# Performance work log

Hardware: AMD Instinct MI355X
Metric: run time of the kernel (lower is better)

The kernel has to match this reference:

```python
import jax, jax.numpy as jnp
import numpy as np

B, N, D = 8, 1024, 1024

def setup_inputs() -> dict:
    key = jax.random.key(0)
    k1, k2, k3, k4, k5 = jax.random.split(key, 5)
    x = jax.random.normal(k1, (B, N, D), dtype=jnp.float32)
    y = jax.random.normal(k2, (B, N, D), dtype=jnp.float32)
    adj = jax.random.uniform(k3, (B, N, N), dtype=jnp.float32)
    adj_sumrow = jnp.sum(adj, axis=-1, keepdims=True)  # [B, N, 1], row-sum normalizer
    W = jax.random.normal(k4, (D, D), dtype=jnp.float32) * (1.0 / np.sqrt(D))
    b = jax.random.normal(k5, (D,), dtype=jnp.float32) * 0.02
    return {"x": x, "y": y, "adj": adj, "adj_sumrow": adj_sumrow, "W": W, "b": b}

def reference(x, y, adj, adj_sumrow, W, b):
    # GraphConvolutionCustom: project neighbor features, aggregate via dense adj,
    # normalize by row-sum, add bias and residual input x; then ReLU.
    # Dropout is identity in eval mode (training=False).
    support = jnp.einsum('bnd,de->bne', y, W)          # [B, N, D]
    agg = jnp.matmul(adj, support) / adj_sumrow        # [B, N, D]
    out = jax.nn.relu(agg + b + x)
    return out
```

## Files before the change

### kernel.cpp

```cpp
#include <hip/hip_runtime.h>
#include <hip/hip_bf16.h>
#include <stdint.h>


typedef float  f32x4  __attribute__((ext_vector_type(4)));
typedef __bf16 bf16x8 __attribute__((ext_vector_type(8)));

__device__ __forceinline__ unsigned short f2bf(float f) {
  union { float f; unsigned int u; } c; c.f = f;
  unsigned int u = c.u;
  u += 0x7FFFu + ((u >> 16) & 1u);
  return (unsigned short)(u >> 16);
}

__device__ __forceinline__ void async_cp16(const void* g, void* l) {
  __builtin_amdgcn_global_load_lds(
      (const __attribute__((address_space(1))) unsigned int*)g,
      (__attribute__((address_space(3))) unsigned int*)l, 16, 0, 0);
}

__device__ __forceinline__ void bar() { asm volatile("s_barrier" ::: "memory"); }
#define VMCNT(n) asm volatile("s_waitcnt vmcnt(" #n ")" ::: "memory")


__global__ __launch_bounds__(256) void k_prep(
    const float4* __restrict__ y4, const float4* __restrict__ a4,
    ushort4* __restrict__ yb, ushort4* __restrict__ ab,
    const float* __restrict__ W, unsigned short* __restrict__ Wt)
{
  __shared__ float t[64][65];
  const int bid = blockIdx.x;
  if (bid < 16384) {
    const int i = bid * 256 + threadIdx.x;
    const bool isY = i < 2097152;
    const float4 v = isY ? y4[i] : a4[i - 2097152];
    ushort4 p;
    p.x = f2bf(v.x); p.y = f2bf(v.y); p.z = f2bf(v.z); p.w = f2bf(v.w);
    if (isY) yb[i] = p; else ab[i - 2097152] = p;
  } else {
    const int id = bid - 16384;
    const int n0 = (id & 15) * 64, k0 = (id >> 4) * 64;
    const int tx = threadIdx.x & 63, ty = threadIdx.x >> 6;
#pragma unroll
    for (int r = ty; r < 64; r += 4)
      t[r][tx] = W[(size_t)(k0 + r) * 1024 + n0 + tx];
    __syncthreads();
#pragma unroll
    for (int r = ty; r < 64; r += 4)
      Wt[(size_t)(n0 + r) * 1024 + k0 + tx] = f2bf(t[tx][r]);
  }
}


__device__ __forceinline__ void stageA(
    const unsigned short* __restrict__ A, int sA, int m0, int k0, int c,
    unsigned short* la, int wave, int rg, int colo)
{
#pragma unroll
  for (int s = 0; s < 2; ++s) {
    const int t = wave * 2 + s;
    const int row0 = (t >> 2) * 64 + c * 32 + (t & 3) * 8;
    async_cp16(A + (size_t)(m0 + row0 + rg) * sA + k0 + colo, la + row0 * 64);
  }
}

__device__ __forceinline__ void stageB(
    const unsigned short* __restrict__ Bt, int sB, int n0, int k0,
    unsigned short* lb, int wave, int rg, int colo)
{
#pragma unroll
  for (int s = 0; s < 2; ++s) {
    const int t = wave * 2 + s;
    const int row0 = t * 8;
    async_cp16(Bt + (size_t)(n0 + row0 + rg) * sB + k0 + colo, lb + row0 * 64);
  }
}

__device__ __forceinline__ void readA(
    const unsigned short* la, bf16x8 af[2][2], int wm, int mh, int quad, int l16)
{
#pragma unroll
  for (int h = 0; h < 2; ++h)
#pragma unroll
    for (int i = 0; i < 2; ++i) {
      const int r = wm + mh * 32 + i * 16 + l16;
      af[h][i] = *(const bf16x8*)(la + r * 64 + ((h * 4 + quad + r) & 7) * 8);
    }
}

__device__ __forceinline__ void readB(
    const unsigned short* lb, bf16x8 bfr[2][2], int wn, int nh, int quad, int l16)
{
#pragma unroll
  for (int h = 0; h < 2; ++h)
#pragma unroll
    for (int j = 0; j < 2; ++j) {
      const int r = wn + nh * 32 + j * 16 + l16;
      bfr[h][j] = *(const bf16x8*)(lb + r * 64 + ((h * 4 + quad + r) & 7) * 8);
    }
}

__device__ __forceinline__ void quad8(
    bf16x8 af[2][2], bf16x8 bfr[2][2], f32x4 acc[4][4], int mh, int nh)
{
  __builtin_amdgcn_s_setprio(1);
#pragma unroll
  for (int h = 0; h < 2; ++h)
#pragma unroll
    for (int i = 0; i < 2; ++i)
#pragma unroll
      for (int j = 0; j < 2; ++j)
        acc[mh * 2 + i][nh * 2 + j] = __builtin_amdgcn_mfma_f32_16x16x32_bf16(
            af[h][i], bfr[h][j], acc[mh * 2 + i][nh * 2 + j], 0, 0, 0);
  __builtin_amdgcn_s_setprio(0);
}

__device__ __forceinline__ void gemm256x128(
    const unsigned short* __restrict__ A,  int sA,
    const unsigned short* __restrict__ Bt, int sB,
    int m0, int n0, f32x4 acc[4][4], unsigned short* lsm, int tid)
{
  const int lane = tid & 63, wave = tid >> 6;
  const int wm = (wave >> 1) * 64, wn = (wave & 1) * 64;
  const int quad = lane >> 4, l16 = lane & 15;
  const int rg = lane >> 3;
  const int colo = (((lane & 7) - rg) & 7) * 8;

  bf16x8 af[2][2], bfr[2][2];

  stageA(A, sA, m0, 0, 0, lsm, wave, rg, colo);
  stageB(Bt, sB, n0, 0, lsm + 16384, wave, rg, colo);
  stageA(A, sA, m0, 0, 1, lsm, wave, rg, colo);

#pragma unroll 1
  for (int T = 0; T < 15; ++T) {
    const unsigned short* la = lsm + (T & 1) * 24576;
    const unsigned short* lb = la + 16384;
    unsigned short* na = lsm + ((T + 1) & 1) * 24576;
    unsigned short* nb = na + 16384;
    const int nk = (T + 1) * 64;

    stageA(A, sA, m0, nk, 0, na, wave, rg, colo);
    VMCNT(4); bar();
    readA(la, af, wm, 0, quad, l16);
    readB(lb, bfr, wn, 0, quad, l16);
    quad8(af, bfr, acc, 0, 0);

    stageB(Bt, sB, n0, nk, nb, wave, rg, colo);
    readB(lb, bfr, wn, 1, quad, l16);
    quad8(af, bfr, acc, 0, 1);

    stageA(A, sA, m0, nk, 1, na, wave, rg, colo);
    VMCNT(6); bar();
    readA(la, af, wm, 1, quad, l16);
    quad8(af, bfr, acc, 1, 1);

    readB(lb, bfr, wn, 0, quad, l16);
    quad8(af, bfr, acc, 1, 0);
  }

  {
    const unsigned short* la = lsm + 24576;
    const unsigned short* lb = la + 16384;
    VMCNT(2); bar();
    readA(la, af, wm, 0, quad, l16);
    readB(lb, bfr, wn, 0, quad, l16);
    quad8(af, bfr, acc, 0, 0);
    readB(lb, bfr, wn, 1, quad, l16);
    quad8(af, bfr, acc, 0, 1);
    VMCNT(0); bar();
    readA(la, af, wm, 1, quad, l16);
    quad8(af, bfr, acc, 1, 1);
    readB(lb, bfr, wn, 0, quad, l16);
    quad8(af, bfr, acc, 1, 0);
  }
}

__device__ __forceinline__ void zero_acc(f32x4 acc[4][4]) {
#pragma unroll
  for (int i = 0; i < 4; ++i)
#pragma unroll
    for (int j = 0; j < 4; ++j)
#pragma unroll
      for (int r = 0; r < 4; ++r) acc[i][j][r] = 0.0f;
}


__global__ __launch_bounds__(512, 2) void k_gemm1(
    const unsigned short* __restrict__ Wt,
    const unsigned short* __restrict__ Ybf,
    unsigned short* __restrict__ Sup2)
{
  __shared__ __align__(16) unsigned short lsm[49152];
  const int tid = threadIdx.x;
  const int xcd = blockIdx.x & 7, slot = blockIdx.x >> 3;
  const int m0 = (slot >> 3) * 256;
  const int n0 = (xcd * 8 + (slot & 7)) * 128;

  f32x4 acc[4][4];
  zero_acc(acc);
  gemm256x128(Wt, 1024, Ybf, 1024, m0, n0, acc, lsm, tid);

  const int lane = tid & 63, wave = tid >> 6;
  const int wm = (wave >> 1) * 64, wn = (wave & 1) * 64;
  const int quad = lane >> 4, l16 = lane & 15;
#pragma unroll
  for (int mi = 0; mi < 4; ++mi) {
    const int mb = m0 + wm + mi * 16 + quad * 4;
#pragma unroll
    for (int r = 0; r < 4; ++r) {
      unsigned short* row = Sup2 + ((size_t)(mb + r) << 13);
#pragma unroll
      for (int nj = 0; nj < 4; ++nj)
        row[n0 + wn + nj * 16 + l16] = f2bf(acc[mi][nj][r]);
    }
  }
}


__global__ __launch_bounds__(512, 2) void k_gemm2(
    const unsigned short* __restrict__ AdjBf,
    const unsigned short* __restrict__ Sup2,
    const float* __restrict__ x,
    const float* __restrict__ sumrow,
    const float* __restrict__ bias,
    float* __restrict__ out)
{
  __shared__ __align__(16) unsigned short lsm[49152];
  const int tid = threadIdx.x;
  const int b = blockIdx.x & 7, slot = blockIdx.x >> 3;
  const int m0 = (slot >> 3) * 256, n0 = (slot & 7) * 128;

  f32x4 acc[4][4];
  zero_acc(acc);
  gemm256x128(AdjBf + ((size_t)b << 20), 1024,
              Sup2 + ((size_t)b << 10), 8192,
              m0, n0, acc, lsm, tid);

  const float* xb = x   + ((size_t)b << 20);
  float*       ob = out + ((size_t)b << 20);
  const float* sr = sumrow + ((size_t)b << 10);
  const int lane = tid & 63, wave = tid >> 6;
  const int wm = (wave >> 1) * 64, wn = (wave & 1) * 64;
  const int quad = lane >> 4, l16 = lane & 15;

  float bv[4];
#pragma unroll
  for (int nj = 0; nj < 4; ++nj) bv[nj] = bias[n0 + wn + nj * 16 + l16];

#pragma unroll
  for (int mi = 0; mi < 4; ++mi) {
    const int mb = m0 + wm + mi * 16 + quad * 4;
#pragma unroll
    for (int r = 0; r < 4; ++r) {
      const int m = mb + r;
      const float inv = 1.0f / sr[m];
#pragma unroll
      for (int nj = 0; nj < 4; ++nj) {
        const int n = n0 + wn + nj * 16 + l16;
        const size_t idx = (((size_t)m) << 10) + n;
        float v = acc[mi][nj][r] * inv + bv[nj] + xb[idx];
        ob[idx] = fmaxf(v, 0.0f);
      }
    }
  }
}


extern "C" void kernel_launch(void* const* d_in, const int* in_sizes, int n_in,
                              void* d_out, int out_size, void* d_ws, size_t ws_size,
                              hipStream_t stream) {
  const float* x      = (const float*)d_in[0];
  const float* y      = (const float*)d_in[1];
  const float* adj    = (const float*)d_in[2];
  const float* sumrow = (const float*)d_in[3];
  const float* W      = (const float*)d_in[4];
  const float* bias   = (const float*)d_in[5];
  float* out = (float*)d_out;

  char* ws = (char*)d_ws;
  unsigned short* ybf   = (unsigned short*)(ws);
  unsigned short* adjbf = (unsigned short*)(ws + ((size_t)16 << 20));
  unsigned short* wt    = (unsigned short*)(ws + ((size_t)32 << 20));
  unsigned short* sup2  = (unsigned short*)(ws + ((size_t)34 << 20));

  k_prep<<<dim3(16640), dim3(256), 0, stream>>>(
      (const float4*)y, (const float4*)adj, (ushort4*)ybf, (ushort4*)adjbf, W, wt);
  k_gemm1<<<dim3(256), dim3(512), 0, stream>>>(wt, ybf, sup2);
  k_gemm2<<<dim3(256), dim3(512), 0, stream>>>(adjbf, sup2, x, sumrow, bias, out);
}
```

Baseline: 195.7 us.

## Switch GEMM mainloop to triple-buffered LDS pipeline with two-phase MFMA schedule

Replaces the double-buffered 256x128 GEMM mainloop with a three-buffer LDS rotation that prefetches two K-tiles ahead. Each wave now loads all four A fragments at once and issues two 16-MFMA phases per tile instead of four 8-MFMA quads, with barriers around each phase. The goal is to hide global-load latency and cut the number of LDS read points per tile. In exchange, LDS per block grows from 96KB to 144KB, which likely limits occupancy to one block per CU despite launch_bounds(512,2), and it adds more barriers per iteration.

```diff
diff --git a/kernel.cpp b/kernel.cpp
--- a/kernel.cpp
+++ b/kernel.cpp
@@ -59,7 +59,7 @@
 #pragma unroll
   for (int s = 0; s < 2; ++s) {
     const int t = wave * 2 + s;
-    const int row0 = (t >> 2) * 64 + c * 32 + (t & 3) * 8;
+    const int row0 = c * 128 + t * 8;
     async_cp16(A + (size_t)(m0 + row0 + rg) * sA + k0 + colo, la + row0 * 64);
   }
 }
@@ -77,13 +77,13 @@
 }
 
 __device__ __forceinline__ void readA(
-    const unsigned short* la, bf16x8 af[2][2], int wm, int mh, int quad, int l16)
+    const unsigned short* la, bf16x8 af[2][4], int wm, int quad, int l16)
 {
 #pragma unroll
   for (int h = 0; h < 2; ++h)
 #pragma unroll
-    for (int i = 0; i < 2; ++i) {
-      const int r = wm + mh * 32 + i * 16 + l16;
+    for (int i = 0; i < 4; ++i) {
+      const int r = wm + i * 16 + l16;
       af[h][i] = *(const bf16x8*)(la + r * 64 + ((h * 4 + quad + r) & 7) * 8);
     }
 }
@@ -100,22 +100,22 @@
     }
 }
 
-__device__ __forceinline__ void quad8(
-    bf16x8 af[2][2], bf16x8 bfr[2][2], f32x4 acc[4][4], int mh, int nh)
+__device__ __forceinline__ void phase16(
+    bf16x8 af[2][4], bf16x8 bfr[2][2], f32x4 acc[4][4], int nh)
 {
   __builtin_amdgcn_s_setprio(1);
 #pragma unroll
   for (int h = 0; h < 2; ++h)
 #pragma unroll
-    for (int i = 0; i < 2; ++i)
+    for (int i = 0; i < 4; ++i)
 #pragma unroll
       for (int j = 0; j < 2; ++j)
-        acc[mh * 2 + i][nh * 2 + j] = __builtin_amdgcn_mfma_f32_16x16x32_bf16(
-            af[h][i], bfr[h][j], acc[mh * 2 + i][nh * 2 + j], 0, 0, 0);
+        acc[i][nh * 2 + j] = __builtin_amdgcn_mfma_f32_16x16x32_bf16(
+            af[h][i], bfr[h][j], acc[i][nh * 2 + j], 0, 0, 0);
   __builtin_amdgcn_s_setprio(0);
 }
 
-__device__ __forceinline__ void gemm256x128(
+__device__ __forceinline__ void gemm_3buf(
     const unsigned short* __restrict__ A,  int sA,
     const unsigned short* __restrict__ Bt, int sB,
     int m0, int n0, f32x4 acc[4][4], unsigned short* lsm, int tid)
@@ -126,53 +126,44 @@
   const int rg = lane >> 3;
   const int colo = (((lane & 7) - rg) & 7) * 8;
 
-  bf16x8 af[2][2], bfr[2][2];
-
-  stageA(A, sA, m0, 0, 0, lsm, wave, rg, colo);
-  stageB(Bt, sB, n0, 0, lsm + 16384, wave, rg, colo);
-  stageA(A, sA, m0, 0, 1, lsm, wave, rg, colo);
+  unsigned short* cur = lsm;
+  unsigned short* nxt = lsm + 24576;
+  unsigned short* stg = lsm + 49152;
+
+  bf16x8 af[2][4], bfr[2][2];
+
+  stageA(A, sA, m0, 0, 0, cur, wave, rg, colo);
+  stageA(A, sA, m0, 0, 1, cur, wave, rg, colo);
+  stageB(Bt, sB, n0, 0, cur + 16384, wave, rg, colo);
+  stageA(A, sA, m0, 64, 0, nxt, wave, rg, colo);
+  stageA(A, sA, m0, 64, 1, nxt, wave, rg, colo);
+  stageB(Bt, sB, n0, 64, nxt + 16384, wave, rg, colo);
+  VMCNT(6);
+  bar();
 
 #pragma unroll 1
-  for (int T = 0; T < 15; ++T) {
-    const unsigned short* la = lsm + (T & 1) * 24576;
-    const unsigned short* lb = la + 16384;
-    unsigned short* na = lsm + ((T + 1) & 1) * 24576;
-    unsigned short* nb = na + 16384;
-    const int nk = (T + 1) * 64;
-
-    stageA(A, sA, m0, nk, 0, na, wave, rg, colo);
-    VMCNT(4); bar();
-    readA(la, af, wm, 0, quad, l16);
-    readB(lb, bfr, wn, 0, quad, l16);
-    quad8(af, bfr, acc, 0, 0);
-
-    stageB(Bt, sB, n0, nk, nb, wave, rg, colo);
-    readB(lb, bfr, wn, 1, quad, l16);
-    quad8(af, bfr, acc, 0, 1);
-
-    stageA(A, sA, m0, nk, 1, na, wave, rg, colo);
-    VMCNT(6); bar();
-    readA(la, af, wm, 1, quad, l16);
-    quad8(af, bfr, acc, 1, 1);
-
-    readB(lb, bfr, wn, 0, quad, l16);
-    quad8(af, bfr, acc, 1, 0);
-  }
-
-  {
-    const unsigned short* la = lsm + 24576;
-    const unsigned short* lb = la + 16384;
-    VMCNT(2); bar();
-    readA(la, af, wm, 0, quad, l16);
-    readB(lb, bfr, wn, 0, quad, l16);
-    quad8(af, bfr, acc, 0, 0);
-    readB(lb, bfr, wn, 1, quad, l16);
-    quad8(af, bfr, acc, 0, 1);
-    VMCNT(0); bar();
-    readA(la, af, wm, 1, quad, l16);
-    quad8(af, bfr, acc, 1, 1);
-    readB(lb, bfr, wn, 0, quad, l16);
-    quad8(af, bfr, acc, 1, 0);
+  for (int T = 0; T < 16; ++T) {
+    const int nk = (T + 2) * 64;
+
+    if (T < 14) stageA(A, sA, m0, nk, 0, stg, wave, rg, colo);
+    readA(cur, af, wm, quad, l16);
+    readB(cur + 16384, bfr, wn, 0, quad, l16);
+    bar();
+    phase16(af, bfr, acc, 0);
+    bar();
+
+    if (T < 14) {
+      stageA(A, sA, m0, nk, 1, stg, wave, rg, colo);
+      stageB(Bt, sB, n0, nk, stg + 16384, wave, rg, colo);
+    }
+    readB(cur + 16384, bfr, wn, 1, quad, l16);
+    if (T < 14)       { VMCNT(6); }
+    else if (T == 14) { VMCNT(0); }
+    bar();
+    phase16(af, bfr, acc, 1);
+    bar();
+
+    unsigned short* tmp = cur; cur = nxt; nxt = stg; stg = tmp;
   }
 }
 
@@ -191,7 +182,7 @@
     const unsigned short* __restrict__ Ybf,
     unsigned short* __restrict__ Sup2)
 {
-  __shared__ __align__(16) unsigned short lsm[49152];
+  __shared__ __align__(16) unsigned short lsm[73728];
   const int tid = threadIdx.x;
   const int xcd = blockIdx.x & 7, slot = blockIdx.x >> 3;
   const int m0 = (slot >> 3) * 256;
@@ -199,7 +190,7 @@
 
   f32x4 acc[4][4];
   zero_acc(acc);
-  gemm256x128(Wt, 1024, Ybf, 1024, m0, n0, acc, lsm, tid);
+  gemm_3buf(Wt, 1024, Ybf, 1024, m0, n0, acc, lsm, tid);
 
   const int lane = tid & 63, wave = tid >> 6;
   const int wm = (wave >> 1) * 64, wn = (wave & 1) * 64;
@@ -226,16 +217,16 @@
     const float* __restrict__ bias,
     float* __restrict__ out)
 {
-  __shared__ __align__(16) unsigned short lsm[49152];
+  __shared__ __align__(16) unsigned short lsm[73728];
   const int tid = threadIdx.x;
   const int b = blockIdx.x & 7, slot = blockIdx.x >> 3;
   const int m0 = (slot >> 3) * 256, n0 = (slot & 7) * 128;
 
   f32x4 acc[4][4];
   zero_acc(acc);
-  gemm256x128(AdjBf + ((size_t)b << 20), 1024,
-              Sup2 + ((size_t)b << 10), 8192,
-              m0, n0, acc, lsm, tid);
+  gemm_3buf(AdjBf + ((size_t)b << 20), 1024,
+            Sup2 + ((size_t)b << 10), 8192,
+            m0, n0, acc, lsm, tid);
 
   const float* xb = x   + ((size_t)b << 20);
   float*       ob = out + ((size_t)b << 20);
```

New measurement: 200.7 us. 1.03x slower.
